# Kernel optimization log

Hardware: AMD Instinct MI355X
Metric: run time of the kernel (lower is better)

## Reference

```python
import jax, jax.numpy as jnp
import numpy as np
from functools import partial

H = 51

def lstm_cell(x, h, c, W_ih, W_hh, b_ih, b_hh):
    # PyTorch LSTMCell: gates ordered (i, f, g, o)
    z = x @ W_ih.T + b_ih + h @ W_hh.T + b_hh  # [B, 4H]
    i, f, g, o = jnp.split(z, 4, axis=-1)
    i = jax.nn.sigmoid(i)
    f = jax.nn.sigmoid(f)
    g = jnp.tanh(g)
    o = jax.nn.sigmoid(o)
    c_new = f * c + i * g
    h_new = o * jnp.tanh(c_new)
    return h_new, c_new


def setup_inputs() -> dict:
    key = jax.random.key(0)
    ks = jax.random.split(key, 12)
    B, T = 2048, 512
    s = 1.0 / np.sqrt(H)  # PyTorch default init scale
    inp = {
        "input": jax.random.normal(ks[0], (B, T), dtype=jnp.float32),
        "W_ih1": jax.random.uniform(ks[1], (4 * H, 1), jnp.float32, -s, s),
        "W_hh1": jax.random.uniform(ks[2], (4 * H, H), jnp.float32, -s, s),
        "b_ih1": jax.random.uniform(ks[3], (4 * H,), jnp.float32, -s, s),
        "b_hh1": jax.random.uniform(ks[4], (4 * H,), jnp.float32, -s, s),
        "W_ih2": jax.random.uniform(ks[5], (4 * H, H), jnp.float32, -s, s),
        "W_hh2": jax.random.uniform(ks[6], (4 * H, H), jnp.float32, -s, s),
        "b_ih2": jax.random.uniform(ks[7], (4 * H,), jnp.float32, -s, s),
        "b_hh2": jax.random.uniform(ks[8], (4 * H,), jnp.float32, -s, s),
        "W_lin": jax.random.uniform(ks[9], (1, H), jnp.float32, -s, s),
        "b_lin": jax.random.uniform(ks[10], (1,), jnp.float32, -s, s),
        "future": 32,
    }
    return inp


def reference(input, W_ih1, W_hh1, b_ih1, b_hh1, W_ih2, W_hh2, b_ih2, b_hh2, W_lin, b_lin, future):
    B, T = input.shape
    dt = input.dtype
    h1 = jnp.zeros((B, H), dt)
    c1 = jnp.zeros((B, H), dt)
    h2 = jnp.zeros((B, H), dt)
    c2 = jnp.zeros((B, H), dt)

    def core(carry, x_t):
        h1, c1, h2, c2 = carry
        h1, c1 = lstm_cell(x_t, h1, c1, W_ih1, W_hh1, b_ih1, b_hh1)
        h2, c2 = lstm_cell(h1, h2, c2, W_ih2, W_hh2, b_ih2, b_hh2)
        out = h2 @ W_lin.T + b_lin  # [B, 1]
        return (h1, c1, h2, c2), out

    xs = input.T[:, :, None]  # [T, B, 1]
    carry, outs = jax.lax.scan(core, (h1, c1, h2, c2), xs)

    def fstep(carry, _):
        state, out = carry
        new_state, new_out = core(state, out)
        return (new_state, new_out), new_out

    last_out = outs[-1]
    _, fouts = jax.lax.scan(fstep, (carry, last_out), None, length=future)

    all_outs = jnp.concatenate([outs, fouts], axis=0)  # [T+future, B, 1]
    return all_outs[:, :, 0].T  # [B, T+future]
```

## Files before the change

### kernel.cpp

```cpp
#include <hip/hip_runtime.h>

#define H 51
#define TIN 512
#define TTOT 544
#define BTILE 8
#define AST 72
#define H2ST 13
#define SOST 548

typedef __attribute__((ext_vector_type(8))) short short8;
typedef __attribute__((ext_vector_type(4))) float float4v;

#define MFMA __builtin_amdgcn_mfma_f32_16x16x32_bf16

__device__ __forceinline__ float fast_rcp(float x) { return __builtin_amdgcn_rcpf(x); }
__device__ __forceinline__ float sigf(float x)  { return fast_rcp(1.0f + __expf(-x)); }
__device__ __forceinline__ float tanhf_(float x){ return 1.0f - 2.0f * fast_rcp(1.0f + __expf(2.0f * x)); }

__device__ __forceinline__ unsigned short bf16rnd(float x) {
    unsigned int u = __float_as_uint(x);
    return (unsigned short)((u + 0x7fffu + ((u >> 16) & 1u)) >> 16);
}
__device__ __forceinline__ void bf16split(float x, unsigned short& hi, float& lo) {
    unsigned int u  = __float_as_uint(x);
    unsigned int hr = (u + 0x7fffu + ((u >> 16) & 1u)) & 0xffff0000u;
    hi = (unsigned short)(hr >> 16);
    lo = x - __uint_as_float(hr);
}

__device__ __forceinline__ float b1val(int k, int u, int g,
                                       const float* Whh1, const float* Wih1) {
    if (u >= H) return 0.0f;
    const int r = g * H + u;
    if (k < H)  return Whh1[r * H + k];
    if (k == H) return Wih1[r];
    return 0.0f;
}
__device__ __forceinline__ float b2val(int k, int u, int g,
                                       const float* Wih2, const float* Whh2) {
    if (u >= H) return 0.0f;
    const int r = g * H + u;
    if (k < H) return Wih2[r * H + k];
    if (k >= 64 && k < 64 + H) return Whh2[r * H + (k - 64)];
    return 0.0f;
}

__global__ __launch_bounds__(512)
__attribute__((amdgpu_waves_per_eu(2, 2)))
void lstm_seq(
    const float* __restrict__ input,
    const float* __restrict__ W_ih1,
    const float* __restrict__ W_hh1,
    const float* __restrict__ b_ih1,
    const float* __restrict__ b_hh1,
    const float* __restrict__ W_ih2,
    const float* __restrict__ W_hh2,
    const float* __restrict__ b_ih2,
    const float* __restrict__ b_hh2,
    const float* __restrict__ W_lin,
    const float* __restrict__ b_lin,
    float* __restrict__ out)
{
    __shared__ __align__(16) unsigned short sA1h[2][16][AST];
    __shared__ __align__(16) unsigned short sA2h[2][16][AST];
    __shared__ float sH2f[2][64][H2ST];
    __shared__ __align__(8) float sXlo[2][8];
    __shared__ float sWlin[64];
    __shared__ __align__(16) float sIn[BTILE][TIN];
    __shared__ __align__(16) float sOut[BTILE][SOST];

    const int tid  = threadIdx.x;
    const int lane = tid & 63;
    const int wv   = tid >> 6;
    const int Lw   = wv >> 2;
    const int ut   = wv & 3;
    const int quad = lane >> 4;
    const int kq   = quad * 8;
    const int nl   = lane & 15;
    const int u    = ut * 16 + nl;
    const int ur   = (u < H) ? u : (H - 1);
    const int b0   = blockIdx.x * BTILE;
    const float blin = b_lin[0];
    const int rowA = (quad & 1) * 4 + (quad >> 1) * 2;
    const int arow = quad * 4;
    const int kc   = lane & 31;
    const int bhead= 2 * ut + (lane >> 5);

    {
        unsigned short* p0 = &sA1h[0][0][0];
        unsigned short* p2 = &sA2h[0][0][0];
        for (int i = tid; i < 2 * 16 * AST; i += 512) { p0[i] = 0; p2[i] = 0; }
        float* pf = &sH2f[0][0][0];
        for (int i = tid; i < 2 * 64 * H2ST; i += 512) pf[i] = 0.0f;
        if (tid < 16) sXlo[tid >> 3][tid & 7] = 0.0f;
        if (tid < 64) sWlin[tid] = (tid < H) ? W_lin[tid] : 0.0f;
        const int r = tid >> 6, l = tid & 63;
        const float* src = input + (size_t)(b0 + r) * TIN;
        *(float4v*)&sIn[r][l * 4]       = *(const float4v*)&src[l * 4];
        *(float4v*)&sIn[r][256 + l * 4] = *(const float4v*)&src[256 + l * 4];
    }
    __syncthreads();
    if (tid < 8) {
        unsigned short hh; float lo;
        bf16split(sIn[tid][0], hh, lo);
        sA1h[0][(tid & 2) ? tid + 6 : tid][51] = hh;
        sXlo[0][tid] = lo;
    }
    __syncthreads();

    if (Lw == 0) {
        short8 B1h[4][2];
        float zb1[4], wxf[4];
        #pragma unroll
        for (int g = 0; g < 4; ++g) {
            #pragma unroll
            for (int kt = 0; kt < 2; ++kt)
                #pragma unroll
                for (int j = 0; j < 8; ++j)
                    B1h[g][kt][j] = (short)bf16rnd(b1val(kt * 32 + kq + j, u, g, W_hh1, W_ih1));
            const int r = g * H + ur;
            zb1[g] = b_ih1[r] + b_hh1[r];
            wxf[g] = W_ih1[r];
        }
        float c1[2] = {0, 0};

        auto l1work = [&](int rs, int ws) __attribute__((always_inline)) {
            short8 a0h = *(const short8*)&sA1h[rs][nl][kq];
            short8 a1h = *(const short8*)&sA1h[rs][nl][32 + kq];
            float2 xl = *(const float2*)&sXlo[rs][rowA];
            float4v C[4];
            #pragma unroll
            for (int g = 0; g < 4; ++g) {
                float4v c = {zb1[g], zb1[g], zb1[g], zb1[g]};
                c = MFMA(a0h, B1h[g][0], c, 0, 0, 0);
                c = MFMA(a1h, B1h[g][1], c, 0, 0, 0);
                C[g] = c;
            }
            float h1v[2];
            #pragma unroll
            for (int j = 0; j < 2; ++j) {
                const float xr = j ? xl.y : xl.x;
                float I = sigf  (C[0][j] + wxf[0] * xr);
                float F = sigf  (C[1][j] + wxf[1] * xr);
                float G = tanhf_(C[2][j] + wxf[2] * xr);
                float O = sigf  (C[3][j] + wxf[3] * xr);
                c1[j] = F * c1[j] + I * G;
                h1v[j] = O * tanhf_(c1[j]);
            }
            if (u < H) {
                #pragma unroll
                for (int j = 0; j < 2; ++j)
                    sA1h[ws][arow + j][u] = bf16rnd(h1v[j]);
            }
        };
        auto headw = [&](int slot, int outt) __attribute__((always_inline)) -> float {
            float p = sWlin[kc]      * sH2f[slot][kc][bhead]
                    + sWlin[kc + 32] * sH2f[slot][kc + 32][bhead];
            p += __shfl_xor(p, 1);  p += __shfl_xor(p, 2);  p += __shfl_xor(p, 4);
            p += __shfl_xor(p, 8);  p += __shfl_xor(p, 16);
            float val = p + blin;
            if (kc == 0) sOut[bhead][outt] = val;
            return val;
        };
        auto teach = [&](int s, int rs, int ws) __attribute__((always_inline)) {
            float xpre = 0.0f;
            const bool doX = (wv == 1) && (lane < 8) && (s + 1 < TIN);
            if (doX) xpre = sIn[lane][s + 1];
            if (s >= 2) headw(ws, s - 2);
            l1work(rs, ws);
            if (doX) {
                unsigned short hh; float lo; bf16split(xpre, hh, lo);
                sA1h[ws][(lane & 2) ? lane + 6 : lane][51] = hh;
                sXlo[ws][lane] = lo;
            }
            __syncthreads();
        };

        for (int s = 0; s < TIN; ++s) {
            if ((s & 1) == 0) teach(s, 0, 1);
            else              teach(s, 1, 0);
        }
        for (int s = TIN; s <= TTOT; ++s) {
            const int rs = s & 1, ws = rs ^ 1;
            __syncthreads();
            {
                float val = headw(rs, s - 1);
                if (kc == 0) {
                    unsigned short hh; float lo; bf16split(val, hh, lo);
                    sA1h[rs][(bhead & 2) ? bhead + 6 : bhead][51] = hh;
                    sXlo[rs][bhead] = lo;
                }
                if (s == TIN) headw(ws, s - 2);
            }
            __syncthreads();
            if (s < TTOT) l1work(rs, ws);
            __syncthreads();
        }
    } else {
        short8 B2h[4][4];
        float zb2[4];
        #pragma unroll
        for (int g = 0; g < 4; ++g) {
            #pragma unroll
            for (int kt = 0; kt < 4; ++kt)
                #pragma unroll
                for (int j = 0; j < 8; ++j)
                    B2h[g][kt][j] = (short)bf16rnd(b2val(kt * 32 + kq + j, u, g, W_ih2, W_hh2));
            const int r = g * H + ur;
            zb2[g] = b_ih2[r] + b_hh2[r];
        }
        float c2[2] = {0, 0};

        auto l2work = [&](int rs, int ws) __attribute__((always_inline)) {
            short8 f0h = *(const short8*)&sA1h[rs][nl][kq];
            short8 f1h = *(const short8*)&sA1h[rs][nl][32 + kq];
            short8 f2h = *(const short8*)&sA2h[rs][nl][kq];
            short8 f3h = *(const short8*)&sA2h[rs][nl][32 + kq];
            float4v C[4];
            #pragma unroll
            for (int g = 0; g < 4; ++g) {
                float4v c = {zb2[g], zb2[g], zb2[g], zb2[g]};
                c = MFMA(f0h, B2h[g][0], c, 0, 0, 0);
                c = MFMA(f1h, B2h[g][1], c, 0, 0, 0);
                c = MFMA(f2h, B2h[g][2], c, 0, 0, 0);
                c = MFMA(f3h, B2h[g][3], c, 0, 0, 0);
                C[g] = c;
            }
            float h2v[2];
            #pragma unroll
            for (int j = 0; j < 2; ++j) {
                float I = sigf  (C[0][j]);
                float F = sigf  (C[1][j]);
                float G = tanhf_(C[2][j]);
                float O = sigf  (C[3][j]);
                c2[j] = F * c2[j] + I * G;
                h2v[j] = O * tanhf_(c2[j]);
            }
            if (u < H) {
                #pragma unroll
                for (int j = 0; j < 2; ++j) {
                    sA2h[ws][arow + j][u] = bf16rnd(h2v[j]);
                    sH2f[rs][u][rowA + j] = h2v[j];
                }
            }
        };

        for (int s = 0; s < TIN; ++s) {
            if ((s & 1) == 0) { if (s) l2work(0, 1); }
            else              l2work(1, 0);
            __syncthreads();
        }
        for (int s = TIN; s <= TTOT; ++s) {
            const int rs = s & 1, ws = rs ^ 1;
            l2work(rs, ws);
            __syncthreads();
            __syncthreads();
            __syncthreads();
        }
    }

    __syncthreads();
    for (int i = tid; i < BTILE * (TTOT / 4); i += 512) {
        const int r = i / (TTOT / 4);
        const int c = i - r * (TTOT / 4);
        *(float4v*)&out[(size_t)(b0 + r) * TTOT + c * 4] =
            *(const float4v*)&sOut[r][c * 4];
    }
}

extern "C" void kernel_launch(void* const* d_in, const int* in_sizes, int n_in,
                              void* d_out, int out_size, void* d_ws, size_t ws_size,
                              hipStream_t stream) {
    const float* input = (const float*)d_in[0];
    const float* W_ih1 = (const float*)d_in[1];
    const float* W_hh1 = (const float*)d_in[2];
    const float* b_ih1 = (const float*)d_in[3];
    const float* b_hh1 = (const float*)d_in[4];
    const float* W_ih2 = (const float*)d_in[5];
    const float* W_hh2 = (const float*)d_in[6];
    const float* b_ih2 = (const float*)d_in[7];
    const float* b_hh2 = (const float*)d_in[8];
    const float* b_lin = (const float*)d_in[10];
    const float* W_lin = (const float*)d_in[9];
    float* out = (float*)d_out;

    lstm_seq<<<dim3(256), dim3(512), 0, stream>>>(input, W_ih1, W_hh1, b_ih1, b_hh1,
                                                  W_ih2, W_hh2, b_ih2, b_hh2,
                                                  W_lin, b_lin, out);
}
```

Measured before the change: 465.5 us.

## Halve batch tile to four rows per block and double grid size

Each block now processes 4 batch rows instead of 8, so the grid doubles to 512 blocks and each lane handles one MFMA output row instead of two, which shortens per-step gate math. The occupancy hint rises to 4 waves per EU so two blocks can share a CU and hide the latency of the serial recurrence. The cost is that MFMA rows are only a quarter utilized, so total matrix work per useful row doubles, and register pressure must fit the higher occupancy target.

```diff
diff --git a/kernel.cpp b/kernel.cpp
--- a/kernel.cpp
+++ b/kernel.cpp
@@ -3,9 +3,9 @@
 #define H 51
 #define TIN 512
 #define TTOT 544
-#define BTILE 8
+#define BTILE 4
 #define AST 72
-#define H2ST 13
+#define H2ST 5
 #define SOST 548
 
 typedef __attribute__((ext_vector_type(8))) short short8;
@@ -46,7 +46,7 @@
 }
 
 __global__ __launch_bounds__(512)
-__attribute__((amdgpu_waves_per_eu(2, 2)))
+__attribute__((amdgpu_waves_per_eu(4, 4)))
 void lstm_seq(
     const float* __restrict__ input,
     const float* __restrict__ W_ih1,
@@ -64,7 +64,7 @@
     __shared__ __align__(16) unsigned short sA1h[2][16][AST];
     __shared__ __align__(16) unsigned short sA2h[2][16][AST];
     __shared__ float sH2f[2][64][H2ST];
-    __shared__ __align__(8) float sXlo[2][8];
+    __shared__ __align__(8) float sXlo[2][BTILE];
     __shared__ float sWlin[64];
     __shared__ __align__(16) float sIn[BTILE][TIN];
     __shared__ __align__(16) float sOut[BTILE][SOST];
@@ -81,10 +81,10 @@
     const int ur   = (u < H) ? u : (H - 1);
     const int b0   = blockIdx.x * BTILE;
     const float blin = b_lin[0];
-    const int rowA = (quad & 1) * 4 + (quad >> 1) * 2;
     const int arow = quad * 4;
     const int kc   = lane & 31;
     const int bhead= 2 * ut + (lane >> 5);
+    const bool headok = (bhead < BTILE);
 
     {
         unsigned short* p0 = &sA1h[0][0][0];
@@ -92,18 +92,17 @@
         for (int i = tid; i < 2 * 16 * AST; i += 512) { p0[i] = 0; p2[i] = 0; }
         float* pf = &sH2f[0][0][0];
         for (int i = tid; i < 2 * 64 * H2ST; i += 512) pf[i] = 0.0f;
-        if (tid < 16) sXlo[tid >> 3][tid & 7] = 0.0f;
+        if (tid < 2 * BTILE) sXlo[tid >> 2][tid & 3] = 0.0f;
         if (tid < 64) sWlin[tid] = (tid < H) ? W_lin[tid] : 0.0f;
-        const int r = tid >> 6, l = tid & 63;
+        const int r = tid >> 7, l = tid & 127;
         const float* src = input + (size_t)(b0 + r) * TIN;
-        *(float4v*)&sIn[r][l * 4]       = *(const float4v*)&src[l * 4];
-        *(float4v*)&sIn[r][256 + l * 4] = *(const float4v*)&src[256 + l * 4];
+        *(float4v*)&sIn[r][l * 4] = *(const float4v*)&src[l * 4];
     }
     __syncthreads();
-    if (tid < 8) {
+    if (tid < BTILE) {
         unsigned short hh; float lo;
         bf16split(sIn[tid][0], hh, lo);
-        sA1h[0][(tid & 2) ? tid + 6 : tid][51] = hh;
+        sA1h[0][4 * tid][51] = hh;
         sXlo[0][tid] = lo;
     }
     __syncthreads();
@@ -122,12 +121,12 @@
             zb1[g] = b_ih1[r] + b_hh1[r];
             wxf[g] = W_ih1[r];
         }
-        float c1[2] = {0, 0};
+        float c1 = 0.0f;
 
         auto l1work = [&](int rs, int ws) __attribute__((always_inline)) {
             short8 a0h = *(const short8*)&sA1h[rs][nl][kq];
             short8 a1h = *(const short8*)&sA1h[rs][nl][32 + kq];
-            float2 xl = *(const float2*)&sXlo[rs][rowA];
+            float xr = sXlo[rs][quad];
             float4v C[4];
             #pragma unroll
             for (int g = 0; g < 4; ++g) {
@@ -136,41 +135,35 @@
                 c = MFMA(a1h, B1h[g][1], c, 0, 0, 0);
                 C[g] = c;
             }
-            float h1v[2];
-            #pragma unroll
-            for (int j = 0; j < 2; ++j) {
-                const float xr = j ? xl.y : xl.x;
-                float I = sigf  (C[0][j] + wxf[0] * xr);
-                float F = sigf  (C[1][j] + wxf[1] * xr);
-                float G = tanhf_(C[2][j] + wxf[2] * xr);
-                float O = sigf  (C[3][j] + wxf[3] * xr);
-                c1[j] = F * c1[j] + I * G;
-                h1v[j] = O * tanhf_(c1[j]);
-            }
-            if (u < H) {
-                #pragma unroll
-                for (int j = 0; j < 2; ++j)
-                    sA1h[ws][arow + j][u] = bf16rnd(h1v[j]);
-            }
+            float I = sigf  (C[0][0] + wxf[0] * xr);
+            float F = sigf  (C[1][0] + wxf[1] * xr);
+            float G = tanhf_(C[2][0] + wxf[2] * xr);
+            float O = sigf  (C[3][0] + wxf[3] * xr);
+            c1 = F * c1 + I * G;
+            float h1v = O * tanhf_(c1);
+            if (u < H) sA1h[ws][arow][u] = bf16rnd(h1v);
         };
         auto headw = [&](int slot, int outt) __attribute__((always_inline)) -> float {
-            float p = sWlin[kc]      * sH2f[slot][kc][bhead]
-                    + sWlin[kc + 32] * sH2f[slot][kc + 32][bhead];
-            p += __shfl_xor(p, 1);  p += __shfl_xor(p, 2);  p += __shfl_xor(p, 4);
-            p += __shfl_xor(p, 8);  p += __shfl_xor(p, 16);
-            float val = p + blin;
-            if (kc == 0) sOut[bhead][outt] = val;
+            float val = 0.0f;
+            if (headok) {
+                float p = sWlin[kc]      * sH2f[slot][kc][bhead]
+                        + sWlin[kc + 32] * sH2f[slot][kc + 32][bhead];
+                p += __shfl_xor(p, 1);  p += __shfl_xor(p, 2);  p += __shfl_xor(p, 4);
+                p += __shfl_xor(p, 8);  p += __shfl_xor(p, 16);
+                val = p + blin;
+                if (kc == 0) sOut[bhead][outt] = val;
+            }
             return val;
         };
         auto teach = [&](int s, int rs, int ws) __attribute__((always_inline)) {
             float xpre = 0.0f;
-            const bool doX = (wv == 1) && (lane < 8) && (s + 1 < TIN);
+            const bool doX = (wv == 1) && (lane < BTILE) && (s + 1 < TIN);
             if (doX) xpre = sIn[lane][s + 1];
             if (s >= 2) headw(ws, s - 2);
             l1work(rs, ws);
             if (doX) {
                 unsigned short hh; float lo; bf16split(xpre, hh, lo);
-                sA1h[ws][(lane & 2) ? lane + 6 : lane][51] = hh;
+                sA1h[ws][4 * lane][51] = hh;
                 sXlo[ws][lane] = lo;
             }
             __syncthreads();
@@ -185,9 +178,9 @@
             __syncthreads();
             {
                 float val = headw(rs, s - 1);
-                if (kc == 0) {
+                if (headok && kc == 0) {
                     unsigned short hh; float lo; bf16split(val, hh, lo);
-                    sA1h[rs][(bhead & 2) ? bhead + 6 : bhead][51] = hh;
+                    sA1h[rs][4 * bhead][51] = hh;
                     sXlo[rs][bhead] = lo;
                 }
                 if (s == TIN) headw(ws, s - 2);
@@ -209,7 +202,7 @@
             const int r = g * H + ur;
             zb2[g] = b_ih2[r] + b_hh2[r];
         }
-        float c2[2] = {0, 0};
+        float c2 = 0.0f;
 
         auto l2work = [&](int rs, int ws) __attribute__((always_inline)) {
             short8 f0h = *(const short8*)&sA1h[rs][nl][kq];
@@ -226,22 +219,15 @@
                 c = MFMA(f3h, B2h[g][3], c, 0, 0, 0);
                 C[g] = c;
             }
-            float h2v[2];
-            #pragma unroll
-            for (int j = 0; j < 2; ++j) {
-                float I = sigf  (C[0][j]);
-                float F = sigf  (C[1][j]);
-                float G = tanhf_(C[2][j]);
-                float O = sigf  (C[3][j]);
-                c2[j] = F * c2[j] + I * G;
-                h2v[j] = O * tanhf_(c2[j]);
-            }
+            float I = sigf  (C[0][0]);
+            float F = sigf  (C[1][0]);
+            float G = tanhf_(C[2][0]);
+            float O = sigf  (C[3][0]);
+            c2 = F * c2 + I * G;
+            float h2v = O * tanhf_(c2);
             if (u < H) {
-                #pragma unroll
-                for (int j = 0; j < 2; ++j) {
-                    sA2h[ws][arow + j][u] = bf16rnd(h2v[j]);
-                    sH2f[rs][u][rowA + j] = h2v[j];
-                }
+                sA2h[ws][arow][u] = bf16rnd(h2v);
+                sH2f[rs][u][quad] = h2v;
             }
         };
 
@@ -280,11 +266,11 @@
     const float* W_hh2 = (const float*)d_in[6];
     const float* b_ih2 = (const float*)d_in[7];
     const float* b_hh2 = (const float*)d_in[8];
+    const float* W_lin = (const float*)d_in[9];
     const float* b_lin = (const float*)d_in[10];
-    const float* W_lin = (const float*)d_in[9];
     float* out = (float*)d_out;
 
-    lstm_seq<<<dim3(256), dim3(512), 0, stream>>>(input, W_ih1, W_hh1, b_ih1, b_hh1,
+    lstm_seq<<<dim3(512), dim3(512), 0, stream>>>(input, W_ih1, W_hh1, b_ih1, b_hh1,
                                                   W_ih2, W_hh2, b_ih2, b_hh2,
                                                   W_lin, b_lin, out);
 }
```

After: 503.8 us. +8.2%, slower.

## Move output head and input staging to dedicated waves, pack bf16 stores

Applied to the files above, without the earlier changes.

Grows the block from 8 to 12 waves. Four extra waves now run the linear output head and stage the next teacher-forced input, so layer-1 waves only do their MFMA and gate work each step. Also packs the two bf16 hidden-state conversions into one v_cvt_pk_bf16_f32 instruction. The aim is to take the head reduction and x-prep off the layer-1 critical path. The cost is more waves at each barrier and lower occupancy per CU (waves_per_eu set to 3).

```diff
diff --git a/kernel.cpp b/kernel.cpp
--- a/kernel.cpp
+++ b/kernel.cpp
@@ -7,6 +7,7 @@
 #define AST 72
 #define H2ST 13
 #define SOST 548
+#define NTHR 768
 
 typedef __attribute__((ext_vector_type(8))) short short8;
 typedef __attribute__((ext_vector_type(4))) float float4v;
@@ -20,6 +21,11 @@
 __device__ __forceinline__ unsigned short bf16rnd(float x) {
     unsigned int u = __float_as_uint(x);
     return (unsigned short)((u + 0x7fffu + ((u >> 16) & 1u)) >> 16);
+}
+__device__ __forceinline__ unsigned int bf16pk(float a, float b) {
+    unsigned int r;
+    asm("v_cvt_pk_bf16_f32 %0, %1, %2" : "=v"(r) : "v"(a), "v"(b));
+    return r;
 }
 __device__ __forceinline__ void bf16split(float x, unsigned short& hi, float& lo) {
     unsigned int u  = __float_as_uint(x);
@@ -45,8 +51,8 @@
     return 0.0f;
 }
 
-__global__ __launch_bounds__(512)
-__attribute__((amdgpu_waves_per_eu(2, 2)))
+__global__ __launch_bounds__(NTHR)
+__attribute__((amdgpu_waves_per_eu(3, 3)))
 void lstm_seq(
     const float* __restrict__ input,
     const float* __restrict__ W_ih1,
@@ -72,7 +78,6 @@
     const int tid  = threadIdx.x;
     const int lane = tid & 63;
     const int wv   = tid >> 6;
-    const int Lw   = wv >> 2;
     const int ut   = wv & 3;
     const int quad = lane >> 4;
     const int kq   = quad * 8;
@@ -89,15 +94,16 @@
     {
         unsigned short* p0 = &sA1h[0][0][0];
         unsigned short* p2 = &sA2h[0][0][0];
-        for (int i = tid; i < 2 * 16 * AST; i += 512) { p0[i] = 0; p2[i] = 0; }
+        for (int i = tid; i < 2 * 16 * AST; i += NTHR) { p0[i] = 0; p2[i] = 0; }
         float* pf = &sH2f[0][0][0];
-        for (int i = tid; i < 2 * 64 * H2ST; i += 512) pf[i] = 0.0f;
+        for (int i = tid; i < 2 * 64 * H2ST; i += NTHR) pf[i] = 0.0f;
         if (tid < 16) sXlo[tid >> 3][tid & 7] = 0.0f;
         if (tid < 64) sWlin[tid] = (tid < H) ? W_lin[tid] : 0.0f;
-        const int r = tid >> 6, l = tid & 63;
-        const float* src = input + (size_t)(b0 + r) * TIN;
-        *(float4v*)&sIn[r][l * 4]       = *(const float4v*)&src[l * 4];
-        *(float4v*)&sIn[r][256 + l * 4] = *(const float4v*)&src[256 + l * 4];
+        for (int i = tid; i < BTILE * (TIN / 4); i += NTHR) {
+            const int r = i >> 7, c = i & 127;
+            *(float4v*)&sIn[r][c * 4] =
+                *(const float4v*)&input[(size_t)(b0 + r) * TIN + c * 4];
+        }
     }
     __syncthreads();
     if (tid < 8) {
@@ -108,7 +114,7 @@
     }
     __syncthreads();
 
-    if (Lw == 0) {
+    if (wv < 4) {
         short8 B1h[4][2];
         float zb1[4], wxf[4];
         #pragma unroll
@@ -148,11 +154,86 @@
                 h1v[j] = O * tanhf_(c1[j]);
             }
             if (u < H) {
+                const unsigned int pk = bf16pk(h1v[0], h1v[1]);
+                sA1h[ws][arow][u]     = (unsigned short)pk;
+                sA1h[ws][arow + 1][u] = (unsigned short)(pk >> 16);
+            }
+        };
+
+        for (int s = 0; s < TIN; ++s) {
+            if ((s & 1) == 0) l1work(0, 1);
+            else              l1work(1, 0);
+            __syncthreads();
+        }
+        for (int s = TIN; s <= TTOT; ++s) {
+            const int rs = s & 1, ws = rs ^ 1;
+            __syncthreads();
+            __syncthreads();
+            if (s < TTOT) l1work(rs, ws);
+            __syncthreads();
+        }
+    } else if (wv < 8) {
+        short8 B2h[4][4];
+        float zb2[4];
+        #pragma unroll
+        for (int g = 0; g < 4; ++g) {
+            #pragma unroll
+            for (int kt = 0; kt < 4; ++kt)
                 #pragma unroll
-                for (int j = 0; j < 2; ++j)
-                    sA1h[ws][arow + j][u] = bf16rnd(h1v[j]);
+                for (int j = 0; j < 8; ++j)
+                    B2h[g][kt][j] = (short)bf16rnd(b2val(kt * 32 + kq + j, u, g, W_ih2, W_hh2));
+            const int r = g * H + ur;
+            zb2[g] = b_ih2[r] + b_hh2[r];
+        }
+        float c2[2] = {0, 0};
+
+        auto l2work = [&](int rs, int ws) __attribute__((always_inline)) {
+            short8 f0h = *(const short8*)&sA1h[rs][nl][kq];
+            short8 f1h = *(const short8*)&sA1h[rs][nl][32 + kq];
+            short8 f2h = *(const short8*)&sA2h[rs][nl][kq];
+            short8 f3h = *(const short8*)&sA2h[rs][nl][32 + kq];
+            float4v C[4];
+            #pragma unroll
+            for (int g = 0; g < 4; ++g) {
+                float4v c = {zb2[g], zb2[g], zb2[g], zb2[g]};
+                c = MFMA(f0h, B2h[g][0], c, 0, 0, 0);
+                c = MFMA(f1h, B2h[g][1], c, 0, 0, 0);
+                c = MFMA(f2h, B2h[g][2], c, 0, 0, 0);
+                c = MFMA(f3h, B2h[g][3], c, 0, 0, 0);
+                C[g] = c;
+            }
+            float h2v[2];
+            #pragma unroll
+            for (int j = 0; j < 2; ++j) {
+                float I = sigf  (C[0][j]);
+                float F = sigf  (C[1][j]);
+                float G = tanhf_(C[2][j]);
+                float O = sigf  (C[3][j]);
+                c2[j] = F * c2[j] + I * G;
+                h2v[j] = O * tanhf_(c2[j]);
+            }
+            if (u < H) {
+                const unsigned int pk = bf16pk(h2v[0], h2v[1]);
+                sA2h[ws][arow][u]     = (unsigned short)pk;
+                sA2h[ws][arow + 1][u] = (unsigned short)(pk >> 16);
+                sH2f[rs][u][rowA]     = h2v[0];
+                sH2f[rs][u][rowA + 1] = h2v[1];
             }
         };
+
+        for (int s = 0; s < TIN; ++s) {
+            if ((s & 1) == 0) { if (s) l2work(0, 1); }
+            else              l2work(1, 0);
+            __syncthreads();
+        }
+        for (int s = TIN; s <= TTOT; ++s) {
+            const int rs = s & 1, ws = rs ^ 1;
+            l2work(rs, ws);
+            __syncthreads();
+            __syncthreads();
+            __syncthreads();
+        }
+    } else {
         auto headw = [&](int slot, int outt) __attribute__((always_inline)) -> float {
             float p = sWlin[kc]      * sH2f[slot][kc][bhead]
                     + sWlin[kc + 32] * sH2f[slot][kc + 32][bhead];
@@ -162,30 +243,23 @@
             if (kc == 0) sOut[bhead][outt] = val;
             return val;
         };
-        auto teach = [&](int s, int rs, int ws) __attribute__((always_inline)) {
-            float xpre = 0.0f;
-            const bool doX = (wv == 1) && (lane < 8) && (s + 1 < TIN);
-            if (doX) xpre = sIn[lane][s + 1];
+
+        for (int s = 0; s < TIN; ++s) {
+            const int ws = (s & 1) ? 0 : 1;
             if (s >= 2) headw(ws, s - 2);
-            l1work(rs, ws);
-            if (doX) {
-                unsigned short hh; float lo; bf16split(xpre, hh, lo);
+            if ((wv == 8) && (lane < 8) && (s + 1 < TIN)) {
+                unsigned short hh; float lo; bf16split(sIn[lane][s + 1], hh, lo);
                 sA1h[ws][(lane & 2) ? lane + 6 : lane][51] = hh;
                 sXlo[ws][lane] = lo;
             }
             __syncthreads();
-        };
-
-        for (int s = 0; s < TIN; ++s) {
-            if ((s & 1) == 0) teach(s, 0, 1);
-            else              teach(s, 1, 0);
         }
         for (int s = TIN; s <= TTOT; ++s) {
             const int rs = s & 1, ws = rs ^ 1;
             __syncthreads();
             {
                 float val = headw(rs, s - 1);
-                if (kc == 0) {
+                if (kc == 0 && s < TTOT) {
                     unsigned short hh; float lo; bf16split(val, hh, lo);
                     sA1h[rs][(bhead & 2) ? bhead + 6 : bhead][51] = hh;
                     sXlo[rs][bhead] = lo;
@@ -193,74 +267,12 @@
                 if (s == TIN) headw(ws, s - 2);
             }
             __syncthreads();
-            if (s < TTOT) l1work(rs, ws);
-            __syncthreads();
-        }
-    } else {
-        short8 B2h[4][4];
-        float zb2[4];
-        #pragma unroll
-        for (int g = 0; g < 4; ++g) {
-            #pragma unroll
-            for (int kt = 0; kt < 4; ++kt)
-                #pragma unroll
-                for (int j = 0; j < 8; ++j)
-                    B2h[g][kt][j] = (short)bf16rnd(b2val(kt * 32 + kq + j, u, g, W_ih2, W_hh2));
-            const int r = g * H + ur;
-            zb2[g] = b_ih2[r] + b_hh2[r];
-        }
-        float c2[2] = {0, 0};
-
-        auto l2work = [&](int rs, int ws) __attribute__((always_inline)) {
-            short8 f0h = *(const short8*)&sA1h[rs][nl][kq];
-            short8 f1h = *(const short8*)&sA1h[rs][nl][32 + kq];
-            short8 f2h = *(const short8*)&sA2h[rs][nl][kq];
-            short8 f3h = *(const short8*)&sA2h[rs][nl][32 + kq];
-            float4v C[4];
-            #pragma unroll
-            for (int g = 0; g < 4; ++g) {
-                float4v c = {zb2[g], zb2[g], zb2[g], zb2[g]};
-                c = MFMA(f0h, B2h[g][0], c, 0, 0, 0);
-                c = MFMA(f1h, B2h[g][1], c, 0, 0, 0);
-                c = MFMA(f2h, B2h[g][2], c, 0, 0, 0);
-                c = MFMA(f3h, B2h[g][3], c, 0, 0, 0);
-                C[g] = c;
-            }
-            float h2v[2];
-            #pragma unroll
-            for (int j = 0; j < 2; ++j) {
-                float I = sigf  (C[0][j]);
-                float F = sigf  (C[1][j]);
-                float G = tanhf_(C[2][j]);
-                float O = sigf  (C[3][j]);
-                c2[j] = F * c2[j] + I * G;
-                h2v[j] = O * tanhf_(c2[j]);
-            }
-            if (u < H) {
-                #pragma unroll
-                for (int j = 0; j < 2; ++j) {
-                    sA2h[ws][arow + j][u] = bf16rnd(h2v[j]);
-                    sH2f[rs][u][rowA + j] = h2v[j];
-                }
-            }
-        };
-
-        for (int s = 0; s < TIN; ++s) {
-            if ((s & 1) == 0) { if (s) l2work(0, 1); }
-            else              l2work(1, 0);
-            __syncthreads();
-        }
-        for (int s = TIN; s <= TTOT; ++s) {
-            const int rs = s & 1, ws = rs ^ 1;
-            l2work(rs, ws);
-            __syncthreads();
-            __syncthreads();
             __syncthreads();
         }
     }
 
     __syncthreads();
-    for (int i = tid; i < BTILE * (TTOT / 4); i += 512) {
+    for (int i = tid; i < BTILE * (TTOT / 4); i += NTHR) {
         const int r = i / (TTOT / 4);
         const int c = i - r * (TTOT / 4);
         *(float4v*)&out[(size_t)(b0 + r) * TTOT + c * 4] =
@@ -280,11 +292,11 @@
     const float* W_hh2 = (const float*)d_in[6];
     const float* b_ih2 = (const float*)d_in[7];
     const float* b_hh2 = (const float*)d_in[8];
+    const float* W_lin = (const float*)d_in[9];
     const float* b_lin = (const float*)d_in[10];
-    const float* W_lin = (const float*)d_in[9];
     float* out = (float*)d_out;
 
-    lstm_seq<<<dim3(256), dim3(512), 0, stream>>>(input, W_ih1, W_hh1, b_ih1, b_hh1,
-                                                  W_ih2, W_hh2, b_ih2, b_hh2,
-                                                  W_lin, b_lin, out);
-}
+    lstm_seq<<<dim3(256), dim3(NTHR), 0, stream>>>(input, W_ih1, W_hh1, b_ih1, b_hh1,
+                                                   W_ih2, W_hh2, b_ih2, b_hh2,
+                                                   W_lin, b_lin, out);
+}
```

Measured after the change: 391.3 us. 1.19x faster.
